# Optimization experiments

Measured on AMD Instinct MI355X. Metric: run time of the kernel, lower is better.

The kernel has to match this reference:

```python
import math
import jax, jax.numpy as jnp
import numpy as np

B, S, H = 4, 2048, 1024

def setup_inputs() -> dict:
    key = jax.random.key(0)
    ks = jax.random.split(key, 7)
    scale = 1.0 / math.sqrt(H)
    return {
        "X":  jax.random.normal(ks[0], (B, S, H), dtype=jnp.float32),
        "Wq": jax.random.normal(ks[1], (H, H), dtype=jnp.float32) * scale,
        "bq": jnp.zeros((H,), dtype=jnp.float32),
        "Wk": jax.random.normal(ks[2], (H, H), dtype=jnp.float32) * scale,
        "bk": jnp.zeros((H,), dtype=jnp.float32),
        "Wv": jax.random.normal(ks[3], (H, H), dtype=jnp.float32) * scale,
        "bv": jnp.zeros((H,), dtype=jnp.float32),
    }

def reference(X, Wq, bq, Wk, bk, Wv, bv):
    # nn.Linear: y = x @ W.T + b
    Q = jnp.einsum("bsh,oh->bso", X, Wq) + bq
    K = jnp.einsum("bsh,oh->bso", X, Wk) + bk
    V = jnp.einsum("bsh,oh->bso", X, Wv) + bv
    hidden_dim = X.shape[-1]
    scores = jnp.einsum("bqh,bkh->bqk", Q, K) / jnp.sqrt(jnp.float32(hidden_dim))
    attn = jax.nn.softmax(scores, axis=-1)  # [B, S, S]
    return jnp.einsum("bqk,bkh->bqh", attn, V)
```

## Files before the change

kernel.cpp:

```cpp
#include <hip/hip_runtime.h>
#include <stdint.h>

#define ASG __attribute__((address_space(1)))
#define ASL __attribute__((address_space(3)))

typedef __bf16 bf16x8 __attribute__((ext_vector_type(8)));
typedef float f32x4 __attribute__((ext_vector_type(4)));

__device__ __forceinline__ unsigned short f2bf(float f) {
  unsigned int u = __builtin_bit_cast(unsigned int, f);
  u = (u + 0x7fffu + ((u >> 16) & 1u)) >> 16;
  return (unsigned short)u;
}

__global__ __launch_bounds__(256) void k_prep(
    const float* __restrict__ X, const float* __restrict__ Wq,
    const float* __restrict__ Wk, const float* __restrict__ Wv,
    const float* __restrict__ bq, const float* __restrict__ bk,
    const float* __restrict__ bv,
    unsigned short* __restrict__ Xb, float* __restrict__ biasF) {
  const int bid = blockIdx.x, tid = threadIdx.x;
  unsigned short* Wb = Xb + 8388608;
  if (bid < 11264) {
    const float* src;
    ushort4* dst;
    int j;
    if (bid < 8192) {
      j = bid * 256 + tid; src = X; dst = (ushort4*)Xb;
    } else {
      int w = (bid - 8192) >> 10;
      j = ((bid - 8192) & 1023) * 256 + tid;
      src = (w == 0) ? Wq : (w == 1 ? Wk : Wv);
      dst = (ushort4*)(Wb + (long)w * 1048576);
    }
    float4 v = reinterpret_cast<const float4*>(src)[j];
    ushort4 o;
    o.x = f2bf(v.x); o.y = f2bf(v.y); o.z = f2bf(v.z); o.w = f2bf(v.w);
    dst[j] = o;
  } else {
    int i = (bid - 11264) * 256 + tid;
    if (i < 3072)
      biasF[i] = (i < 1024) ? bq[i] : (i < 2048 ? bk[i - 1024] : bv[i - 2048]);
  }
}

template <int OUT_MODE, int BIAS>
__global__ __launch_bounds__(512, 2) void gemm3p(
    const unsigned short* __restrict__ A, const unsigned short* __restrict__ B,
    void* __restrict__ Cv, const float* __restrict__ bias,
    int lda, int ldb, int ldc, int K, float alpha,
    long sA, long sB, long sC) {
  __shared__ __align__(16) char smem[147456];
  const int tid = threadIdx.x;
  const int wid = tid >> 6, lane = tid & 63;
  const int wr = wid >> 2, wc = wid & 3;
  const int bm0 = blockIdx.y << 7, bn0 = blockIdx.x << 8;
  A += (long)blockIdx.z * sA;
  B += (long)blockIdx.z * sB;
  const int NT = K >> 6;

  const int srow = tid >> 3;
  const int scol = (((tid & 7) ^ (srow & 7)) << 3);
  long gA[2], gB[4];
#pragma unroll
  for (int u = 0; u < 2; ++u)
    gA[u] = (long)(bm0 + u * 64 + srow) * lda + scol;
#pragma unroll
  for (int u = 0; u < 4; ++u)
    gB[u] = (long)(bn0 + u * 64 + srow) * ldb + scol;

#define STG(PTR, GOFF, KK, LDSOFF)                                             \
  __builtin_amdgcn_global_load_lds((ASG const void*)((PTR) + (GOFF) + ((KK) << 6)), \
      (ASL void*)(smem + (LDSOFF) + wid * 1024), 16, 0, 0)

#define STG_ALL(KK, SB_) do { int kk = (KK); if (kk >= NT) kk -= NT;           \
    STG(A, gA[0], kk, (SB_));                                                  \
    STG(A, gA[1], kk, (SB_) + 8192);                                           \
    STG(B, gB[0], kk, (SB_) + 16384);                                          \
    STG(B, gB[1], kk, (SB_) + 24576);                                          \
    STG(B, gB[2], kk, (SB_) + 32768);                                          \
    STG(B, gB[3], kk, (SB_) + 40960); } while (0)

  const int arow0 = (wr * 64 + (lane & 15)) << 7;
  const int brow0 = 16384 + ((wc * 64 + (lane & 15)) << 7);
  int colk[2];
#pragma unroll
  for (int ks = 0; ks < 2; ++ks)
    colk[ks] = (((ks << 2) + (lane >> 4)) ^ (lane & 7)) << 4;

  bf16x8 afr[4][2];
  bf16x8 b01[2][2];
  bf16x8 b23[2][2];
  f32x4 acc[4][4] = {};

#define RDA(CB) do { _Pragma("unroll") for (int mf = 0; mf < 4; ++mf)          \
    _Pragma("unroll") for (int ks = 0; ks < 2; ++ks)                           \
      afr[mf][ks] = *(const bf16x8*)(smem + (CB) + arow0 + (mf << 11) + colk[ks]); } while (0)
#define RDB01(CB) do { _Pragma("unroll") for (int nf = 0; nf < 2; ++nf)        \
    _Pragma("unroll") for (int ks = 0; ks < 2; ++ks)                           \
      b01[nf][ks] = *(const bf16x8*)(smem + (CB) + brow0 + (nf << 11) + colk[ks]); } while (0)
#define RDB23(CB) do { _Pragma("unroll") for (int nf = 0; nf < 2; ++nf)        \
    _Pragma("unroll") for (int ks = 0; ks < 2; ++ks)                           \
      b23[nf][ks] = *(const bf16x8*)(smem + (CB) + brow0 + ((nf + 2) << 11) + colk[ks]); } while (0)

#define MM(BF, NB) do {                                                        \
    _Pragma("unroll") for (int mf = 0; mf < 4; ++mf)                           \
    _Pragma("unroll") for (int nf = 0; nf < 2; ++nf)                           \
    _Pragma("unroll") for (int ks = 0; ks < 2; ++ks)                           \
      acc[mf][(NB) + nf] = __builtin_amdgcn_mfma_f32_16x16x32_bf16(            \
          afr[mf][ks], BF[nf][ks], acc[mf][(NB) + nf], 0, 0, 0); } while (0)

  STG_ALL(0, 0);
  STG_ALL(1, 49152);
  asm volatile("s_waitcnt vmcnt(6)" ::: "memory");
  __builtin_amdgcn_s_barrier();
  RDA(0); RDB01(0);

  int bc = 0, bs = 2 * 49152;
  for (int t = 0; t < NT; ++t) {
    RDB23(bc);
    STG_ALL(t + 2, bs);
    __builtin_amdgcn_s_setprio(1);
    MM(b01, 0);
    MM(b23, 2);
    __builtin_amdgcn_s_setprio(0);
    asm volatile("s_waitcnt vmcnt(6) lgkmcnt(0)" ::: "memory");
    __builtin_amdgcn_s_barrier();
    const int bn = (bc == 2 * 49152) ? 0 : bc + 49152;
    if (t + 1 < NT) { RDA(bn); RDB01(bn); }
    bc = bn;
    bs = (bs == 2 * 49152) ? 0 : bs + 49152;
  }

  const int r0 = bm0 + wr * 64 + ((lane >> 4) << 2);
  const int c0 = bn0 + wc * 64 + (lane & 15);
#pragma unroll
  for (int mf = 0; mf < 4; ++mf)
#pragma unroll
    for (int nf = 0; nf < 4; ++nf) {
      const int row0 = r0 + mf * 16;
      const int col = c0 + nf * 16;
      f32x4 v = acc[mf][nf];
      const float bb = BIAS ? bias[col] : 0.0f;
      if (OUT_MODE == 0) {
        unsigned short* C = (unsigned short*)Cv + (long)blockIdx.z * sC;
#pragma unroll
        for (int j = 0; j < 4; ++j)
          C[(long)(row0 + j) * ldc + col] = f2bf(v[j] * alpha + bb);
      } else {
        float* C = (float*)Cv + (long)blockIdx.z * sC;
#pragma unroll
        for (int j = 0; j < 4; ++j)
          C[(long)(row0 + j) * ldc + col] = v[j] * alpha + bb;
      }
    }
#undef STG
#undef STG_ALL
#undef RDA
#undef RDB01
#undef RDB23
#undef MM
}

__global__ __launch_bounds__(256) void k_softmax_bf16(unsigned short* __restrict__ S) {
  long row = blockIdx.x;
  unsigned short* R = S + row * 2048;
  int t = threadIdx.x;
  int wid = t >> 6, lane = t & 63;
  uint4 raw = reinterpret_cast<const uint4*>(R)[t];
  unsigned int w[4] = {raw.x, raw.y, raw.z, raw.w};
  float v[8];
#pragma unroll
  for (int j = 0; j < 4; ++j) {
    v[2 * j]     = __builtin_bit_cast(float, (unsigned int)(w[j] << 16));
    v[2 * j + 1] = __builtin_bit_cast(float, (unsigned int)(w[j] & 0xffff0000u));
  }
  float m = v[0];
#pragma unroll
  for (int j = 1; j < 8; ++j) m = fmaxf(m, v[j]);
#pragma unroll
  for (int off = 32; off >= 1; off >>= 1) m = fmaxf(m, __shfl_xor(m, off));
  __shared__ float red[8];
  if (lane == 0) red[wid] = m;
  __syncthreads();
  m = fmaxf(fmaxf(red[0], red[1]), fmaxf(red[2], red[3]));

  float e[8], s = 0.f;
#pragma unroll
  for (int j = 0; j < 8; ++j) { e[j] = __expf(v[j] - m); s += e[j]; }
#pragma unroll
  for (int off = 32; off >= 1; off >>= 1) s += __shfl_xor(s, off);
  if (lane == 0) red[4 + wid] = s;
  __syncthreads();
  s = red[4] + red[5] + red[6] + red[7];
  float inv = 1.0f / s;

  uint4 o;
  unsigned int* ow = &o.x;
#pragma unroll
  for (int j = 0; j < 4; ++j)
    ow[j] = (unsigned int)f2bf(e[2 * j] * inv) |
            ((unsigned int)f2bf(e[2 * j + 1] * inv) << 16);
  reinterpret_cast<uint4*>(R)[t] = o;
}

__global__ __launch_bounds__(256) void k_transpose_v(const unsigned short* __restrict__ V,
                                                     unsigned short* __restrict__ Vt) {
  __shared__ unsigned short tile[32][33];
  int b = blockIdx.z;
  int s0 = blockIdx.y * 32, h0 = blockIdx.x * 32;
  const unsigned short* Vb = V + (long)b * 2048 * 3072;
  unsigned short* Vtb = Vt + (long)b * 1024 * 2048;
  int tx = threadIdx.x & 31, ty = threadIdx.x >> 5;
#pragma unroll
  for (int i = 0; i < 4; ++i)
    tile[ty + 8 * i][tx] = Vb[(long)(s0 + ty + 8 * i) * 3072 + h0 + tx];
  __syncthreads();
#pragma unroll
  for (int i = 0; i < 4; ++i)
    Vtb[(long)(h0 + ty + 8 * i) * 2048 + s0 + tx] = tile[tx][ty + 8 * i];
}

extern "C" void kernel_launch(void* const* d_in, const int* in_sizes, int n_in,
                              void* d_out, int out_size, void* d_ws, size_t ws_size,
                              hipStream_t stream) {
  const float* X  = (const float*)d_in[0];
  const float* Wq = (const float*)d_in[1];
  const float* bq = (const float*)d_in[2];
  const float* Wk = (const float*)d_in[3];
  const float* bk = (const float*)d_in[4];
  const float* Wv = (const float*)d_in[5];
  const float* bv = (const float*)d_in[6];
  float* out = (float*)d_out;
  (void)in_sizes; (void)n_in; (void)out_size; (void)ws_size;

  constexpr long S = 2048, H = 1024;
  constexpr long MS = 4 * S;

  size_t off = 0;
  auto alloc = [&](size_t bytes) { char* p = (char*)d_ws + off; off += bytes; return p; };
  unsigned short* Xb    = (unsigned short*)alloc(MS * H * 2);
  unsigned short* Wb    = (unsigned short*)alloc(3 * H * H * 2);
  float*          biasF = (float*)alloc(3 * H * 4);
  unsigned short* QKVb  = (unsigned short*)alloc(MS * 3 * H * 2);
  unsigned short* Vt    = (unsigned short*)alloc(4 * H * S * 2);
  unsigned short* Sb    = (unsigned short*)alloc(4 * S * S * 2);
  (void)Wb;

  k_prep<<<dim3(11276), 256, 0, stream>>>(X, Wq, Wk, Wv, bq, bk, bv, Xb, biasF);

  gemm3p<0, 1><<<dim3(12, 64, 1), 512, 0, stream>>>(Xb, Xb + MS * H, QKVb, biasF,
                                                    1024, 1024, 3072, 1024, 1.0f, 0, 0, 0);

  gemm3p<0, 0><<<dim3(8, 16, 4), 512, 0, stream>>>(QKVb, QKVb + 1024, Sb, nullptr,
                                                   3072, 3072, 2048, 1024, 0.03125f,
                                                   S * 3 * H, S * 3 * H, S * S);

  k_softmax_bf16<<<dim3((int)MS), 256, 0, stream>>>(Sb);

  k_transpose_v<<<dim3(32, 64, 4), 256, 0, stream>>>(QKVb + 2048, Vt);

  gemm3p<1, 0><<<dim3(4, 16, 4), 512, 0, stream>>>(Sb, Vt, out, nullptr,
                                                   2048, 2048, 1024, 2048, 1.0f,
                                                   S * S, H * S, S * H);
}
```

Baseline: 170.0 us.

## Replace 3-stage GEMM with 256-row tiles and 8-phase interleaved load/MFMA schedule

Replaces the triple-buffered 128xN GEMM with a double-buffered kernel using 256-row M tiles and a templated N width (NF*64). Each K-step is split into quadrant phases that interleave half-tile global-to-LDS loads, LDS fragment reads and MFMA blocks, with barriers and priority bumps between them. Larger tiles are meant to raise data reuse per LDS byte and to hide load latency better. The cost is more accumulator registers, a grid reshaped per GEMM, and many more barriers per iteration.

```diff
diff --git a/kernel.cpp b/kernel.cpp
--- a/kernel.cpp
+++ b/kernel.cpp
@@ -44,100 +44,151 @@
   }
 }
 
-template <int OUT_MODE, int BIAS>
-__global__ __launch_bounds__(512, 2) void gemm3p(
+template <int NF, int OUT_MODE, int BIAS>
+__global__ __launch_bounds__(512, 2) void gemm8p(
     const unsigned short* __restrict__ A, const unsigned short* __restrict__ B,
     void* __restrict__ Cv, const float* __restrict__ bias,
     int lda, int ldb, int ldc, int K, float alpha,
     long sA, long sB, long sC) {
-  __shared__ __align__(16) char smem[147456];
-  const int tid = threadIdx.x;
-  const int wid = tid >> 6, lane = tid & 63;
+  constexpr int QN0 = (NF + 1) / 2, QN1 = NF - QN0;
+  constexpr int BUFSZ = 32768 + NF * 8192;
+  __shared__ __align__(16) char smem[2 * BUFSZ];
+  const int tid = threadIdx.x, wid = tid >> 6, lane = tid & 63;
   const int wr = wid >> 2, wc = wid & 3;
-  const int bm0 = blockIdx.y << 7, bn0 = blockIdx.x << 8;
+  const int bm0 = blockIdx.y << 8, bn0 = blockIdx.x * (NF * 64);
   A += (long)blockIdx.z * sA;
   B += (long)blockIdx.z * sB;
   const int NT = K >> 6;
 
   const int srow = tid >> 3;
-  const int scol = (((tid & 7) ^ (srow & 7)) << 3);
-  long gA[2], gB[4];
-#pragma unroll
-  for (int u = 0; u < 2; ++u)
-    gA[u] = (long)(bm0 + u * 64 + srow) * lda + scol;
-#pragma unroll
-  for (int u = 0; u < 4; ++u)
-    gB[u] = (long)(bn0 + u * 64 + srow) * ldb + scol;
-
-#define STG(PTR, GOFF, KK, LDSOFF)                                             \
-  __builtin_amdgcn_global_load_lds((ASG const void*)((PTR) + (GOFF) + ((KK) << 6)), \
-      (ASL void*)(smem + (LDSOFF) + wid * 1024), 16, 0, 0)
-
-#define STG_ALL(KK, SB_) do { int kk = (KK); if (kk >= NT) kk -= NT;           \
-    STG(A, gA[0], kk, (SB_));                                                  \
-    STG(A, gA[1], kk, (SB_) + 8192);                                           \
-    STG(B, gB[0], kk, (SB_) + 16384);                                          \
-    STG(B, gB[1], kk, (SB_) + 24576);                                          \
-    STG(B, gB[2], kk, (SB_) + 32768);                                          \
-    STG(B, gB[3], kk, (SB_) + 40960); } while (0)
-
-  const int arow0 = (wr * 64 + (lane & 15)) << 7;
-  const int brow0 = 16384 + ((wc * 64 + (lane & 15)) << 7);
+  const int scol = ((tid & 7) ^ (srow & 7)) << 3;
+
+  long srcA_[2][2];
+  int dstA_[2][2];
+#pragma unroll
+  for (int h = 0; h < 2; ++h)
+#pragma unroll
+    for (int j = 0; j < 2; ++j) {
+      srcA_[h][j] = (long)(bm0 + j * 128 + h * 64 + srow) * lda + scol;
+      dstA_[h][j] = h * 16384 + j * 8192;
+    }
+  long srcB_[2][2];
+  int dstB_[2][2];
+  {
+    if constexpr (QN0 == 2) {
+#pragma unroll
+      for (int j = 0; j < 2; ++j) {
+        int u = j * 64 + srow;
+        srcB_[0][j] = (long)(bn0 + (u >> 5) * (NF * 16) + (u & 31)) * ldb + scol;
+        dstB_[0][j] = 32768 + j * 8192;
+      }
+    } else {
+      srcB_[0][0] = (long)(bn0 + (srow >> 4) * (NF * 16) + (srow & 15)) * ldb + scol;
+      dstB_[0][0] = 32768;
+      srcB_[0][1] = srcB_[0][0]; dstB_[0][1] = dstB_[0][0];
+    }
+    if constexpr (QN1 == 2) {
+#pragma unroll
+      for (int j = 0; j < 2; ++j) {
+        int u = j * 64 + srow;
+        srcB_[1][j] = (long)(bn0 + (u >> 5) * (NF * 16) + QN0 * 16 + (u & 31)) * ldb + scol;
+        dstB_[1][j] = 32768 + QN0 * 8192 + j * 8192;
+      }
+    } else {
+      srcB_[1][0] = (long)(bn0 + (srow >> 4) * (NF * 16) + QN0 * 16 + (srow & 15)) * ldb + scol;
+      dstB_[1][0] = 32768 + QN0 * 8192;
+      srcB_[1][1] = srcB_[1][0]; dstB_[1][1] = dstB_[1][0];
+    }
+  }
+
+#define GL(SRC, DST) __builtin_amdgcn_global_load_lds((ASG const void*)(SRC), (ASL void*)(DST), 16, 0, 0)
+#define STG_AH(H, KT, BUF) do { int kk = (KT); if (kk >= NT) kk -= NT; long ko = (long)kk << 6; \
+    GL(A + srcA_[H][0] + ko, smem + (BUF) + dstA_[H][0] + wid * 1024);                          \
+    GL(A + srcA_[H][1] + ko, smem + (BUF) + dstA_[H][1] + wid * 1024); } while (0)
+#define STG_BH(H, KT, BUF) do { int kk = (KT); if (kk >= NT) kk -= NT; long ko = (long)kk << 6; \
+    GL(B + srcB_[H][0] + ko, smem + (BUF) + dstB_[H][0] + wid * 1024);                          \
+    if constexpr (((H) ? QN1 : QN0) == 2)                                                       \
+      GL(B + srcB_[H][1] + ko, smem + (BUF) + dstB_[H][1] + wid * 1024); } while (0)
+
+  const int L = lane & 15;
+  int aoff[8], boff[NF];
+#pragma unroll
+  for (int mf = 0; mf < 8; ++mf) {
+    int row = (mf < 4) ? (wr * 64 + mf * 16 + L) : (128 + wr * 64 + (mf - 4) * 16 + L);
+    aoff[mf] = row << 7;
+  }
+#pragma unroll
+  for (int nf = 0; nf < NF; ++nf) {
+    int row = (nf < QN0) ? (wc * (QN0 * 16) + nf * 16 + L)
+                         : (QN0 * 64 + wc * (QN1 * 16) + (nf - QN0) * 16 + L);
+    boff[nf] = 32768 + (row << 7);
+  }
   int colk[2];
 #pragma unroll
   for (int ks = 0; ks < 2; ++ks)
     colk[ks] = (((ks << 2) + (lane >> 4)) ^ (lane & 7)) << 4;
 
-  bf16x8 afr[4][2];
-  bf16x8 b01[2][2];
-  bf16x8 b23[2][2];
-  f32x4 acc[4][4] = {};
-
-#define RDA(CB) do { _Pragma("unroll") for (int mf = 0; mf < 4; ++mf)          \
-    _Pragma("unroll") for (int ks = 0; ks < 2; ++ks)                           \
-      afr[mf][ks] = *(const bf16x8*)(smem + (CB) + arow0 + (mf << 11) + colk[ks]); } while (0)
-#define RDB01(CB) do { _Pragma("unroll") for (int nf = 0; nf < 2; ++nf)        \
-    _Pragma("unroll") for (int ks = 0; ks < 2; ++ks)                           \
-      b01[nf][ks] = *(const bf16x8*)(smem + (CB) + brow0 + (nf << 11) + colk[ks]); } while (0)
-#define RDB23(CB) do { _Pragma("unroll") for (int nf = 0; nf < 2; ++nf)        \
-    _Pragma("unroll") for (int ks = 0; ks < 2; ++ks)                           \
-      b23[nf][ks] = *(const bf16x8*)(smem + (CB) + brow0 + ((nf + 2) << 11) + colk[ks]); } while (0)
-
-#define MM(BF, NB) do {                                                        \
-    _Pragma("unroll") for (int mf = 0; mf < 4; ++mf)                           \
-    _Pragma("unroll") for (int nf = 0; nf < 2; ++nf)                           \
-    _Pragma("unroll") for (int ks = 0; ks < 2; ++ks)                           \
-      acc[mf][(NB) + nf] = __builtin_amdgcn_mfma_f32_16x16x32_bf16(            \
-          afr[mf][ks], BF[nf][ks], acc[mf][(NB) + nf], 0, 0, 0); } while (0)
-
-  STG_ALL(0, 0);
-  STG_ALL(1, 49152);
-  asm volatile("s_waitcnt vmcnt(6)" ::: "memory");
-  __builtin_amdgcn_s_barrier();
-  RDA(0); RDB01(0);
-
-  int bc = 0, bs = 2 * 49152;
-  for (int t = 0; t < NT; ++t) {
-    RDB23(bc);
-    STG_ALL(t + 2, bs);
-    __builtin_amdgcn_s_setprio(1);
-    MM(b01, 0);
-    MM(b23, 2);
-    __builtin_amdgcn_s_setprio(0);
-    asm volatile("s_waitcnt vmcnt(6) lgkmcnt(0)" ::: "memory");
-    __builtin_amdgcn_s_barrier();
-    const int bn = (bc == 2 * 49152) ? 0 : bc + 49152;
-    if (t + 1 < NT) { RDA(bn); RDB01(bn); }
-    bc = bn;
-    bs = (bs == 2 * 49152) ? 0 : bs + 49152;
-  }
-
-  const int r0 = bm0 + wr * 64 + ((lane >> 4) << 2);
-  const int c0 = bn0 + wc * 64 + (lane & 15);
-#pragma unroll
-  for (int mf = 0; mf < 4; ++mf)
-#pragma unroll
-    for (int nf = 0; nf < 4; ++nf) {
+  bf16x8 afr[8][2];
+  bf16x8 bfr[NF][2];
+  f32x4 acc[8][NF] = {};
+
+#define RDA(BUF, MLO) do { _Pragma("unroll") for (int mf = (MLO); mf < (MLO) + 4; ++mf) \
+    _Pragma("unroll") for (int ks = 0; ks < 2; ++ks)                                    \
+      afr[mf][ks] = *(const bf16x8*)(smem + (BUF) + aoff[mf] + colk[ks]); } while (0)
+#define RDB(BUF, NLO, NHI) do { _Pragma("unroll") for (int nf = (NLO); nf < (NHI); ++nf) \
+    _Pragma("unroll") for (int ks = 0; ks < 2; ++ks)                                     \
+      bfr[nf][ks] = *(const bf16x8*)(smem + (BUF) + boff[nf] + colk[ks]); } while (0)
+#define MMQ(MLO, NLO, NHI) do { _Pragma("unroll") for (int mf = (MLO); mf < (MLO) + 4; ++mf) \
+    _Pragma("unroll") for (int nf = (NLO); nf < (NHI); ++nf)                                 \
+    _Pragma("unroll") for (int ks = 0; ks < 2; ++ks)                                         \
+      acc[mf][nf] = __builtin_amdgcn_mfma_f32_16x16x32_bf16(                                 \
+          afr[mf][ks], bfr[nf][ks], acc[mf][nf], 0, 0, 0); } while (0)
+
+#define BAR() __builtin_amdgcn_s_barrier()
+#define LGKM0() asm volatile("s_waitcnt lgkmcnt(0)" ::: "memory")
+#define VMW() do { if constexpr (QN0 == 2) asm volatile("s_waitcnt vmcnt(6)" ::: "memory"); \
+                   else asm volatile("s_waitcnt vmcnt(5)" ::: "memory"); } while (0)
+#define PRIO1() __builtin_amdgcn_s_setprio(1)
+#define PRIO0() __builtin_amdgcn_s_setprio(0)
+
+  STG_AH(0, 0, 0); STG_AH(1, 0, 0); STG_BH(0, 0, 0); STG_BH(1, 0, 0);
+  STG_AH(0, 1, BUFSZ); STG_AH(1, 1, BUFSZ); STG_BH(0, 1, BUFSZ);
+  VMW();
+  BAR();
+
+  const int NI = NT >> 1;
+  for (int i = 0; i < NI; ++i) {
+    const int t = 2 * i;
+    RDA(0, 0); RDB(0, 0, QN0);
+    STG_BH(1, t + 1, BUFSZ);
+    BAR(); LGKM0(); PRIO1(); MMQ(0, 0, QN0); PRIO0(); BAR();
+    RDA(0, 4);
+    STG_AH(0, t + 2, 0);
+    BAR(); LGKM0(); PRIO1(); MMQ(4, 0, QN0); PRIO0(); BAR();
+    RDB(0, QN0, NF);
+    STG_AH(1, t + 2, 0);
+    BAR(); LGKM0(); PRIO1(); MMQ(0, QN0, NF); PRIO0(); BAR();
+    STG_BH(0, t + 2, 0);
+    BAR(); LGKM0(); PRIO1(); MMQ(4, QN0, NF); PRIO0(); VMW(); BAR();
+    RDA(BUFSZ, 0); RDB(BUFSZ, 0, QN0);
+    STG_BH(1, t + 2, 0);
+    BAR(); LGKM0(); PRIO1(); MMQ(0, 0, QN0); PRIO0(); BAR();
+    RDA(BUFSZ, 4);
+    STG_AH(0, t + 3, BUFSZ);
+    BAR(); LGKM0(); PRIO1(); MMQ(4, 0, QN0); PRIO0(); BAR();
+    RDB(BUFSZ, QN0, NF);
+    STG_AH(1, t + 3, BUFSZ);
+    BAR(); LGKM0(); PRIO1(); MMQ(0, QN0, NF); PRIO0(); BAR();
+    STG_BH(0, t + 3, BUFSZ);
+    BAR(); LGKM0(); PRIO1(); MMQ(4, QN0, NF); PRIO0(); VMW(); BAR();
+  }
+
+  const int r0 = bm0 + wr * 128 + ((lane >> 4) << 2);
+  const int c0 = bn0 + wc * (NF * 16) + (lane & 15);
+#pragma unroll
+  for (int mf = 0; mf < 8; ++mf)
+#pragma unroll
+    for (int nf = 0; nf < NF; ++nf) {
       const int row0 = r0 + mf * 16;
       const int col = c0 + nf * 16;
       f32x4 v = acc[mf][nf];
@@ -154,12 +205,17 @@
           C[(long)(row0 + j) * ldc + col] = v[j] * alpha + bb;
       }
     }
-#undef STG
-#undef STG_ALL
+#undef GL
+#undef STG_AH
+#undef STG_BH
 #undef RDA
-#undef RDB01
-#undef RDB23
-#undef MM
+#undef RDB
+#undef MMQ
+#undef BAR
+#undef LGKM0
+#undef VMW
+#undef PRIO1
+#undef PRIO0
 }
 
 __global__ __launch_bounds__(256) void k_softmax_bf16(unsigned short* __restrict__ S) {
@@ -249,18 +305,18 @@
 
   k_prep<<<dim3(11276), 256, 0, stream>>>(X, Wq, Wk, Wv, bq, bk, bv, Xb, biasF);
 
-  gemm3p<0, 1><<<dim3(12, 64, 1), 512, 0, stream>>>(Xb, Xb + MS * H, QKVb, biasF,
-                                                    1024, 1024, 3072, 1024, 1.0f, 0, 0, 0);
-
-  gemm3p<0, 0><<<dim3(8, 16, 4), 512, 0, stream>>>(QKVb, QKVb + 1024, Sb, nullptr,
-                                                   3072, 3072, 2048, 1024, 0.03125f,
-                                                   S * 3 * H, S * 3 * H, S * S);
+  gemm8p<3, 0, 1><<<dim3(16, 32, 1), 512, 0, stream>>>(Xb, Xb + MS * H, QKVb, biasF,
+                                                       1024, 1024, 3072, 1024, 1.0f, 0, 0, 0);
+
+  gemm8p<4, 0, 0><<<dim3(8, 8, 4), 512, 0, stream>>>(QKVb, QKVb + 1024, Sb, nullptr,
+                                                     3072, 3072, 2048, 1024, 0.03125f,
+                                                     S * 3 * H, S * 3 * H, S * S);
 
   k_softmax_bf16<<<dim3((int)MS), 256, 0, stream>>>(Sb);
 
   k_transpose_v<<<dim3(32, 64, 4), 256, 0, stream>>>(QKVb + 2048, Vt);
 
-  gemm3p<1, 0><<<dim3(4, 16, 4), 512, 0, stream>>>(Sb, Vt, out, nullptr,
-                                                   2048, 2048, 1024, 2048, 1.0f,
-                                                   S * S, H * S, S * H);
-}
+  gemm8p<2, 1, 0><<<dim3(8, 8, 4), 512, 0, stream>>>(Sb, Vt, out, nullptr,
+                                                     2048, 2048, 1024, 2048, 1.0f,
+                                                     S * S, H * S, S * H);
+}
```

New measurement: 233.3 us. 1.37x slower.

## Halve GEMM K-tile to 32 to cut LDS and allow more resident blocks

Applied to the files above, without the earlier changes.

The GEMM K-step drops from 64 to 32, so each of the three pipeline stages needs half the LDS (72KB total instead of 144KB). The staging loads, swizzle pattern, fragment offsets and wait counts are rewritten to match, and the launch bounds now request 4 blocks per CU. The aim is higher occupancy to hide latency, at the cost of twice as many loop iterations and barriers per tile, and possible register pressure from the tighter launch bound.

```diff
diff --git a/kernel.cpp b/kernel.cpp
--- a/kernel.cpp
+++ b/kernel.cpp
@@ -45,78 +45,71 @@
 }
 
 template <int OUT_MODE, int BIAS>
-__global__ __launch_bounds__(512, 2) void gemm3p(
+__global__ __launch_bounds__(512, 4) void gemm3q(
     const unsigned short* __restrict__ A, const unsigned short* __restrict__ B,
     void* __restrict__ Cv, const float* __restrict__ bias,
     int lda, int ldb, int ldc, int K, float alpha,
     long sA, long sB, long sC) {
-  __shared__ __align__(16) char smem[147456];
+  __shared__ __align__(16) char smem[73728];
   const int tid = threadIdx.x;
   const int wid = tid >> 6, lane = tid & 63;
   const int wr = wid >> 2, wc = wid & 3;
   const int bm0 = blockIdx.y << 7, bn0 = blockIdx.x << 8;
   A += (long)blockIdx.z * sA;
   B += (long)blockIdx.z * sB;
-  const int NT = K >> 6;
-
-  const int srow = tid >> 3;
-  const int scol = (((tid & 7) ^ (srow & 7)) << 3);
-  long gA[2], gB[4];
+  const int NT = K >> 5;
+
+  const int srow = tid >> 2;
+  const int scol = (((tid & 3) ^ ((srow >> 1) & 3)) << 3);
+  long gA0, gB[2];
+  gA0 = (long)(bm0 + srow) * lda + scol;
 #pragma unroll
   for (int u = 0; u < 2; ++u)
-    gA[u] = (long)(bm0 + u * 64 + srow) * lda + scol;
-#pragma unroll
-  for (int u = 0; u < 4; ++u)
-    gB[u] = (long)(bn0 + u * 64 + srow) * ldb + scol;
+    gB[u] = (long)(bn0 + u * 128 + srow) * ldb + scol;
 
 #define STG(PTR, GOFF, KK, LDSOFF)                                             \
-  __builtin_amdgcn_global_load_lds((ASG const void*)((PTR) + (GOFF) + ((KK) << 6)), \
+  __builtin_amdgcn_global_load_lds((ASG const void*)((PTR) + (GOFF) + ((KK) << 5)), \
       (ASL void*)(smem + (LDSOFF) + wid * 1024), 16, 0, 0)
 
 #define STG_ALL(KK, SB_) do { int kk = (KK); if (kk >= NT) kk -= NT;           \
-    STG(A, gA[0], kk, (SB_));                                                  \
-    STG(A, gA[1], kk, (SB_) + 8192);                                           \
-    STG(B, gB[0], kk, (SB_) + 16384);                                          \
-    STG(B, gB[1], kk, (SB_) + 24576);                                          \
-    STG(B, gB[2], kk, (SB_) + 32768);                                          \
-    STG(B, gB[3], kk, (SB_) + 40960); } while (0)
-
-  const int arow0 = (wr * 64 + (lane & 15)) << 7;
-  const int brow0 = 16384 + ((wc * 64 + (lane & 15)) << 7);
-  int colk[2];
-#pragma unroll
-  for (int ks = 0; ks < 2; ++ks)
-    colk[ks] = (((ks << 2) + (lane >> 4)) ^ (lane & 7)) << 4;
-
-  bf16x8 afr[4][2];
-  bf16x8 b01[2][2];
-  bf16x8 b23[2][2];
+    STG(A, gA0, kk, (SB_));                                                    \
+    STG(B, gB[0], kk, (SB_) + 8192);                                           \
+    STG(B, gB[1], kk, (SB_) + 16384); } while (0)
+
+  const int L = lane & 15;
+  const int blk = ((lane >> 4) ^ ((L >> 1) & 3)) << 4;
+  int aoff[4], boff[4];
+#pragma unroll
+  for (int mf = 0; mf < 4; ++mf)
+    aoff[mf] = ((wr * 64 + mf * 16 + L) << 6) + blk;
+#pragma unroll
+  for (int nf = 0; nf < 4; ++nf)
+    boff[nf] = 8192 + ((wc * 64 + nf * 16 + L) << 6) + blk;
+
+  bf16x8 afr[4];
+  bf16x8 b01[2], b23[2];
   f32x4 acc[4][4] = {};
 
 #define RDA(CB) do { _Pragma("unroll") for (int mf = 0; mf < 4; ++mf)          \
-    _Pragma("unroll") for (int ks = 0; ks < 2; ++ks)                           \
-      afr[mf][ks] = *(const bf16x8*)(smem + (CB) + arow0 + (mf << 11) + colk[ks]); } while (0)
+      afr[mf] = *(const bf16x8*)(smem + (CB) + aoff[mf]); } while (0)
 #define RDB01(CB) do { _Pragma("unroll") for (int nf = 0; nf < 2; ++nf)        \
-    _Pragma("unroll") for (int ks = 0; ks < 2; ++ks)                           \
-      b01[nf][ks] = *(const bf16x8*)(smem + (CB) + brow0 + (nf << 11) + colk[ks]); } while (0)
+      b01[nf] = *(const bf16x8*)(smem + (CB) + boff[nf]); } while (0)
 #define RDB23(CB) do { _Pragma("unroll") for (int nf = 0; nf < 2; ++nf)        \
-    _Pragma("unroll") for (int ks = 0; ks < 2; ++ks)                           \
-      b23[nf][ks] = *(const bf16x8*)(smem + (CB) + brow0 + ((nf + 2) << 11) + colk[ks]); } while (0)
+      b23[nf] = *(const bf16x8*)(smem + (CB) + boff[nf + 2]); } while (0)
 
 #define MM(BF, NB) do {                                                        \
     _Pragma("unroll") for (int mf = 0; mf < 4; ++mf)                           \
     _Pragma("unroll") for (int nf = 0; nf < 2; ++nf)                           \
-    _Pragma("unroll") for (int ks = 0; ks < 2; ++ks)                           \
       acc[mf][(NB) + nf] = __builtin_amdgcn_mfma_f32_16x16x32_bf16(            \
-          afr[mf][ks], BF[nf][ks], acc[mf][(NB) + nf], 0, 0, 0); } while (0)
+          afr[mf], BF[nf], acc[mf][(NB) + nf], 0, 0, 0); } while (0)
 
   STG_ALL(0, 0);
-  STG_ALL(1, 49152);
-  asm volatile("s_waitcnt vmcnt(6)" ::: "memory");
+  STG_ALL(1, 24576);
+  asm volatile("s_waitcnt vmcnt(3)" ::: "memory");
   __builtin_amdgcn_s_barrier();
   RDA(0); RDB01(0);
 
-  int bc = 0, bs = 2 * 49152;
+  int bc = 0, bs = 2 * 24576;
   for (int t = 0; t < NT; ++t) {
     RDB23(bc);
     STG_ALL(t + 2, bs);
@@ -124,12 +117,12 @@
     MM(b01, 0);
     MM(b23, 2);
     __builtin_amdgcn_s_setprio(0);
-    asm volatile("s_waitcnt vmcnt(6) lgkmcnt(0)" ::: "memory");
+    asm volatile("s_waitcnt vmcnt(3) lgkmcnt(0)" ::: "memory");
     __builtin_amdgcn_s_barrier();
-    const int bn = (bc == 2 * 49152) ? 0 : bc + 49152;
+    const int bn = (bc == 2 * 24576) ? 0 : bc + 24576;
     if (t + 1 < NT) { RDA(bn); RDB01(bn); }
     bc = bn;
-    bs = (bs == 2 * 49152) ? 0 : bs + 49152;
+    bs = (bs == 2 * 24576) ? 0 : bs + 24576;
   }
 
   const int r0 = bm0 + wr * 64 + ((lane >> 4) << 2);
@@ -249,10 +242,10 @@
 
   k_prep<<<dim3(11276), 256, 0, stream>>>(X, Wq, Wk, Wv, bq, bk, bv, Xb, biasF);
 
-  gemm3p<0, 1><<<dim3(12, 64, 1), 512, 0, stream>>>(Xb, Xb + MS * H, QKVb, biasF,
+  gemm3q<0, 1><<<dim3(12, 64, 1), 512, 0, stream>>>(Xb, Xb + MS * H, QKVb, biasF,
                                                     1024, 1024, 3072, 1024, 1.0f, 0, 0, 0);
 
-  gemm3p<0, 0><<<dim3(8, 16, 4), 512, 0, stream>>>(QKVb, QKVb + 1024, Sb, nullptr,
+  gemm3q<0, 0><<<dim3(8, 16, 4), 512, 0, stream>>>(QKVb, QKVb + 1024, Sb, nullptr,
                                                    3072, 3072, 2048, 1024, 0.03125f,
                                                    S * 3 * H, S * 3 * H, S * S);
 
@@ -260,7 +253,7 @@
 
   k_transpose_v<<<dim3(32, 64, 4), 256, 0, stream>>>(QKVb + 2048, Vt);
 
-  gemm3p<1, 0><<<dim3(4, 16, 4), 512, 0, stream>>>(Sb, Vt, out, nullptr,
+  gemm3q<1, 0><<<dim3(4, 16, 4), 512, 0, stream>>>(Sb, Vt, out, nullptr,
                                                    2048, 2048, 1024, 2048, 1.0f,
                                                    S * S, H * S, S * H);
 }
```

Result: slower. 175.1 us (+3.0%).

## Fuse V transpose into QKV GEMM epilogue and add XCD-aware block swizzle

Applied to the files above, without the earlier changes.

The QKV projection GEMM now writes the V slice directly in transposed layout into Vt, so the separate transpose kernel is removed. This eliminates one launch and a read/write pass over V. The attention GEMMs use a 1D grid remapped so each XCD pair works on a single batch, aiming to improve L2 locality. The transposed stores are strided 8-byte writes, which may coalesce poorly.

```diff
diff --git a/kernel.cpp b/kernel.cpp
--- a/kernel.cpp
+++ b/kernel.cpp
@@ -44,19 +44,31 @@
   }
 }
 
-template <int OUT_MODE, int BIAS>
+template <int OUT_MODE, int BIAS, int SWZ>
 __global__ __launch_bounds__(512, 2) void gemm3p(
     const unsigned short* __restrict__ A, const unsigned short* __restrict__ B,
     void* __restrict__ Cv, const float* __restrict__ bias,
+    unsigned short* __restrict__ VtOut, int nx,
     int lda, int ldb, int ldc, int K, float alpha,
     long sA, long sB, long sC) {
   __shared__ __align__(16) char smem[147456];
   const int tid = threadIdx.x;
   const int wid = tid >> 6, lane = tid & 63;
   const int wr = wid >> 2, wc = wid & 3;
-  const int bm0 = blockIdx.y << 7, bn0 = blockIdx.x << 8;
-  A += (long)blockIdx.z * sA;
-  B += (long)blockIdx.z * sB;
+  int bx, by, bz;
+  if constexpr (SWZ) {
+    const int lid = blockIdx.x;
+    const int xcd = lid & 7;
+    bz = xcd >> 1;
+    const int idx = ((lid >> 3) << 1) + (xcd & 1);
+    bx = idx % nx;
+    by = idx / nx;
+  } else {
+    bx = blockIdx.x; by = blockIdx.y; bz = blockIdx.z;
+  }
+  const int bm0 = by << 7, bn0 = bx << 8;
+  A += (long)bz * sA;
+  B += (long)bz * sB;
   const int NT = K >> 6;
 
   const int srow = tid >> 3;
@@ -88,27 +100,26 @@
   for (int ks = 0; ks < 2; ++ks)
     colk[ks] = (((ks << 2) + (lane >> 4)) ^ (lane & 7)) << 4;
 
-  bf16x8 afr[4][2];
-  bf16x8 b01[2][2];
-  bf16x8 b23[2][2];
+  bf16x8 afr2[4][2];
+  bf16x8 b01f[2][2], b23f[2][2];
   f32x4 acc[4][4] = {};
 
 #define RDA(CB) do { _Pragma("unroll") for (int mf = 0; mf < 4; ++mf)          \
     _Pragma("unroll") for (int ks = 0; ks < 2; ++ks)                           \
-      afr[mf][ks] = *(const bf16x8*)(smem + (CB) + arow0 + (mf << 11) + colk[ks]); } while (0)
+      afr2[mf][ks] = *(const bf16x8*)(smem + (CB) + arow0 + (mf << 11) + colk[ks]); } while (0)
 #define RDB01(CB) do { _Pragma("unroll") for (int nf = 0; nf < 2; ++nf)        \
     _Pragma("unroll") for (int ks = 0; ks < 2; ++ks)                           \
-      b01[nf][ks] = *(const bf16x8*)(smem + (CB) + brow0 + (nf << 11) + colk[ks]); } while (0)
+      b01f[nf][ks] = *(const bf16x8*)(smem + (CB) + brow0 + (nf << 11) + colk[ks]); } while (0)
 #define RDB23(CB) do { _Pragma("unroll") for (int nf = 0; nf < 2; ++nf)        \
     _Pragma("unroll") for (int ks = 0; ks < 2; ++ks)                           \
-      b23[nf][ks] = *(const bf16x8*)(smem + (CB) + brow0 + ((nf + 2) << 11) + colk[ks]); } while (0)
+      b23f[nf][ks] = *(const bf16x8*)(smem + (CB) + brow0 + ((nf + 2) << 11) + colk[ks]); } while (0)
 
 #define MM(BF, NB) do {                                                        \
     _Pragma("unroll") for (int mf = 0; mf < 4; ++mf)                           \
     _Pragma("unroll") for (int nf = 0; nf < 2; ++nf)                           \
     _Pragma("unroll") for (int ks = 0; ks < 2; ++ks)                           \
       acc[mf][(NB) + nf] = __builtin_amdgcn_mfma_f32_16x16x32_bf16(            \
-          afr[mf][ks], BF[nf][ks], acc[mf][(NB) + nf], 0, 0, 0); } while (0)
+          afr2[mf][ks], BF[nf][ks], acc[mf][(NB) + nf], 0, 0, 0); } while (0)
 
   STG_ALL(0, 0);
   STG_ALL(1, 49152);
@@ -121,8 +132,8 @@
     RDB23(bc);
     STG_ALL(t + 2, bs);
     __builtin_amdgcn_s_setprio(1);
-    MM(b01, 0);
-    MM(b23, 2);
+    MM(b01f, 0);
+    MM(b23f, 2);
     __builtin_amdgcn_s_setprio(0);
     asm volatile("s_waitcnt vmcnt(6) lgkmcnt(0)" ::: "memory");
     __builtin_amdgcn_s_barrier();
@@ -134,26 +145,45 @@
 
   const int r0 = bm0 + wr * 64 + ((lane >> 4) << 2);
   const int c0 = bn0 + wc * 64 + (lane & 15);
-#pragma unroll
-  for (int mf = 0; mf < 4; ++mf)
-#pragma unroll
-    for (int nf = 0; nf < 4; ++nf) {
+  if (OUT_MODE == 3 && bn0 >= 2048) {
+#pragma unroll
+    for (int mf = 0; mf < 4; ++mf) {
       const int row0 = r0 + mf * 16;
-      const int col = c0 + nf * 16;
-      f32x4 v = acc[mf][nf];
-      const float bb = BIAS ? bias[col] : 0.0f;
-      if (OUT_MODE == 0) {
-        unsigned short* C = (unsigned short*)Cv + (long)blockIdx.z * sC;
-#pragma unroll
-        for (int j = 0; j < 4; ++j)
-          C[(long)(row0 + j) * ldc + col] = f2bf(v[j] * alpha + bb);
-      } else {
-        float* C = (float*)Cv + (long)blockIdx.z * sC;
-#pragma unroll
-        for (int j = 0; j < 4; ++j)
-          C[(long)(row0 + j) * ldc + col] = v[j] * alpha + bb;
+      const int b = row0 >> 11, s = row0 & 2047;
+      unsigned short* Vb = VtOut + (long)b * 2097152;
+#pragma unroll
+      for (int nf = 0; nf < 4; ++nf) {
+        const int col = c0 + nf * 16;
+        const float bb = BIAS ? bias[col] : 0.0f;
+        f32x4 v = acc[mf][nf];
+        ushort4 o;
+        o.x = f2bf(v[0] * alpha + bb); o.y = f2bf(v[1] * alpha + bb);
+        o.z = f2bf(v[2] * alpha + bb); o.w = f2bf(v[3] * alpha + bb);
+        *reinterpret_cast<ushort4*>(Vb + (long)(col - 2048) * 2048 + s) = o;
       }
     }
+  } else {
+#pragma unroll
+    for (int mf = 0; mf < 4; ++mf)
+#pragma unroll
+      for (int nf = 0; nf < 4; ++nf) {
+        const int row0 = r0 + mf * 16;
+        const int col = c0 + nf * 16;
+        f32x4 v = acc[mf][nf];
+        const float bb = BIAS ? bias[col] : 0.0f;
+        if (OUT_MODE == 0 || OUT_MODE == 3) {
+          unsigned short* C = (unsigned short*)Cv + (long)bz * sC;
+#pragma unroll
+          for (int j = 0; j < 4; ++j)
+            C[(long)(row0 + j) * ldc + col] = f2bf(v[j] * alpha + bb);
+        } else {
+          float* C = (float*)Cv + (long)bz * sC;
+#pragma unroll
+          for (int j = 0; j < 4; ++j)
+            C[(long)(row0 + j) * ldc + col] = v[j] * alpha + bb;
+        }
+      }
+  }
 #undef STG
 #undef STG_ALL
 #undef RDA
@@ -202,23 +232,6 @@
     ow[j] = (unsigned int)f2bf(e[2 * j] * inv) |
             ((unsigned int)f2bf(e[2 * j + 1] * inv) << 16);
   reinterpret_cast<uint4*>(R)[t] = o;
-}
-
-__global__ __launch_bounds__(256) void k_transpose_v(const unsigned short* __restrict__ V,
-                                                     unsigned short* __restrict__ Vt) {
-  __shared__ unsigned short tile[32][33];
-  int b = blockIdx.z;
-  int s0 = blockIdx.y * 32, h0 = blockIdx.x * 32;
-  const unsigned short* Vb = V + (long)b * 2048 * 3072;
-  unsigned short* Vtb = Vt + (long)b * 1024 * 2048;
-  int tx = threadIdx.x & 31, ty = threadIdx.x >> 5;
-#pragma unroll
-  for (int i = 0; i < 4; ++i)
-    tile[ty + 8 * i][tx] = Vb[(long)(s0 + ty + 8 * i) * 3072 + h0 + tx];
-  __syncthreads();
-#pragma unroll
-  for (int i = 0; i < 4; ++i)
-    Vtb[(long)(h0 + ty + 8 * i) * 2048 + s0 + tx] = tile[tx][ty + 8 * i];
 }
 
 extern "C" void kernel_launch(void* const* d_in, const int* in_sizes, int n_in,
@@ -249,18 +262,17 @@
 
   k_prep<<<dim3(11276), 256, 0, stream>>>(X, Wq, Wk, Wv, bq, bk, bv, Xb, biasF);
 
-  gemm3p<0, 1><<<dim3(12, 64, 1), 512, 0, stream>>>(Xb, Xb + MS * H, QKVb, biasF,
-                                                    1024, 1024, 3072, 1024, 1.0f, 0, 0, 0);
-
-  gemm3p<0, 0><<<dim3(8, 16, 4), 512, 0, stream>>>(QKVb, QKVb + 1024, Sb, nullptr,
-                                                   3072, 3072, 2048, 1024, 0.03125f,
-                                                   S * 3 * H, S * 3 * H, S * S);
+  gemm3p<3, 1, 0><<<dim3(12, 64, 1), 512, 0, stream>>>(
+      Xb, Xb + MS * H, QKVb, biasF, Vt, 0,
+      1024, 1024, 3072, 1024, 1.0f, 0, 0, 0);
+
+  gemm3p<0, 0, 1><<<dim3(512), 512, 0, stream>>>(
+      QKVb, QKVb + 1024, Sb, nullptr, nullptr, 8,
+      3072, 3072, 2048, 1024, 0.03125f, S * 3 * H, S * 3 * H, S * S);
 
   k_softmax_bf16<<<dim3((int)MS), 256, 0, stream>>>(Sb);
 
-  k_transpose_v<<<dim3(32, 64, 4), 256, 0, stream>>>(QKVb + 2048, Vt);
-
-  gemm3p<1, 0><<<dim3(4, 16, 4), 512, 0, stream>>>(Sb, Vt, out, nullptr,
-                                                   2048, 2048, 1024, 2048, 1.0f,
-                                                   S * S, H * S, S * H);
-}
+  gemm3p<1, 0, 1><<<dim3(256), 512, 0, stream>>>(
+      Sb, Vt, out, nullptr, nullptr, 4,
+      2048, 2048, 1024, 2048, 1.0f, S * S, H * S, S * H);
+}
```

After: 157.9 us. 1.08x faster.
